# Optimization experiments

Hardware: AMD Instinct MI355X
Metric: run time of the kernel (lower is better)

## Reference

```python
import jax, jax.numpy as jnp
import numpy as np

CH_N = 12
CH_N_CONST = 4
CH_E = 8
MAX_V = 100.0
DT = 1.0


def _build_graph(n_inputs, n_hid, n_actions):
    n_nodes = n_inputs + n_hid + n_actions + 1
    mid = np.arange(n_inputs, n_inputs + n_hid + n_actions)
    src = np.concatenate([
        np.repeat(np.arange(n_inputs), n_hid + n_actions),
        np.repeat(np.arange(n_inputs, n_inputs + n_hid), n_hid + n_actions),
        np.full(n_nodes - 1, n_nodes - 1),
    ])
    tgt = np.concatenate([
        np.tile(mid, n_inputs),
        np.tile(mid, n_hid),
        np.arange(n_nodes - 1),
    ])
    return src.astype(np.int32), tgt.astype(np.int32), n_nodes


def setup_inputs() -> dict:
    n_inputs, n_hid, n_actions, B = 64, 1024, 16, 2
    src, tgt, n_nodes = _build_graph(n_inputs, n_hid, n_actions)
    n_edges = src.shape[0]
    key = jax.random.key(0)
    ks = jax.random.split(key, 10)
    s = 0.05
    d_msg_in = 2 + 2 * CH_N + CH_E          # 34
    d_msg_out = 2 * (CH_N - CH_N_CONST) + CH_E  # 24
    d_upd_in = 3 * CH_N - 2 * CH_N_CONST    # 28
    return {
        "nodes": jax.random.normal(ks[0], (B, n_nodes, CH_N), jnp.float32) * s,
        "edges": jax.random.normal(ks[1], (B, n_edges, CH_E), jnp.float32) * s,
        "msg_w1": jax.random.normal(ks[2], (32, d_msg_in), jnp.float32) * s,
        "msg_b1": jax.random.normal(ks[3], (32,), jnp.float32) * s,
        "msg_w2": jax.random.normal(ks[4], (d_msg_out, 32), jnp.float32) * s,
        "msg_b2": jax.random.normal(ks[5], (d_msg_out,), jnp.float32) * s,
        "upd_w1": jax.random.normal(ks[6], (16, d_upd_in), jnp.float32) * s,
        "upd_b1": jax.random.normal(ks[7], (16,), jnp.float32) * s,
        "upd_w2": jax.random.normal(ks[8], (CH_N - CH_N_CONST, 16), jnp.float32) * s,
        "upd_b2": jax.random.normal(ks[9], (CH_N - CH_N_CONST,), jnp.float32) * s,
        "sources": jnp.asarray(src),
        "targets": jnp.asarray(tgt),
    }


def reference(nodes, edges, msg_w1, msg_b1, msg_w2, msg_b2,
              upd_w1, upd_b1, upd_w2, upd_b2, sources, targets):
    B, N, _ = nodes.shape
    E = edges.shape[1]
    d = CH_N - CH_N_CONST  # dynamic node channels = 8

    # degree features (float for concat)
    out_degs = jax.ops.segment_sum(jnp.ones((E,), nodes.dtype), sources, num_segments=N)
    in_degs = jax.ops.segment_sum(jnp.ones((E,), nodes.dtype), targets, num_segments=N)
    od = jnp.broadcast_to(out_degs[sources][None, :, None], (B, E, 1))
    idg = jnp.broadcast_to(in_degs[targets][None, :, None], (B, E, 1))

    # gather + message MLP: [B, E, 34] -> 32 -> 24
    m_x = jnp.concatenate([nodes[:, sources], nodes[:, targets], edges, od, idg], axis=2)
    h = jax.nn.relu(jnp.einsum('bef,hf->beh', m_x, msg_w1) + msg_b1)
    m = jnp.einsum('beh,oh->beo', h, msg_w2) + msg_b2
    m_a, m_b, m_ab = m[..., :d], m[..., d:2 * d], m[..., 2 * d:]

    # scatter-aggregate (mean)
    agg_a = jnp.zeros((B, N, d), m.dtype).at[:, sources].add(m_a)
    agg_b = jnp.zeros((B, N, d), m.dtype).at[:, targets].add(m_b)
    agg_a = agg_a / jnp.maximum(out_degs, 1.0)[None, :, None]
    agg_b = agg_b / jnp.maximum(in_degs, 1.0)[None, :, None]

    # update MLP: [B, N, 28] -> 16 -> 8
    u_x = jnp.concatenate([agg_a, agg_b, nodes], axis=2)
    uh = jax.nn.relu(jnp.einsum('bnf,hf->bnh', u_x, upd_w1) + upd_b1)
    update = jnp.einsum('bnh,oh->bno', uh, upd_w2) + upd_b2

    # node step (decay=0, set_nodes=False, hard clamp)
    new_dyn = jnp.clip(nodes[..., :d] + update * DT, -MAX_V, MAX_V)
    new_nodes = jnp.concatenate([new_dyn, nodes[..., d:]], axis=-1)
    # edge step (ch_e_const=0, hard clamp)
    new_edges = jnp.clip(edges + m_ab * DT, -MAX_V, MAX_V)
    return new_nodes, new_edges
```

## Files before the change

### kernel.cpp

```cpp
#include <hip/hip_runtime.h>
#include <stdint.h>

#define D_IN1 34
#define H1    32
#define D_OUT1 24
#define D_IN2 28
#define H2    16
#define D_OUT2 8
#define CHN   12
#define CHE   8

__device__ __forceinline__ float clip100(float f) { return fminf(fmaxf(f, -100.f), 100.f); }

__global__ void k_zero(int* __restrict__ p, int n_words) {
    int i = blockIdx.x * blockDim.x + threadIdx.x;
    if (i < n_words) p[i] = 0;
}

__global__ void k_degs(const int* __restrict__ src, const int* __restrict__ tgt,
                       int* __restrict__ outd, int* __restrict__ ind, int E, int N) {
    extern __shared__ int hist[];
    int* ho = hist;
    int* hi = hist + N;
    for (int k = threadIdx.x; k < 2 * N; k += blockDim.x) hist[k] = 0;
    __syncthreads();
    for (int e = blockIdx.x * blockDim.x + threadIdx.x; e < E;
         e += gridDim.x * blockDim.x) {
        int s = src[e];
        int t = tgt[e];
        int s0 = __shfl(s, 0);
        unsigned long long act = __ballot(1);
        if (__all(s == s0)) {
            if ((threadIdx.x & 63) == 0) atomicAdd(&ho[s0], (int)__popcll(act));
        } else {
            atomicAdd(&ho[s], 1);
        }
        atomicAdd(&hi[t], 1);
    }
    __syncthreads();
    for (int k = threadIdx.x; k < N; k += blockDim.x) {
        int a = ho[k], b = hi[k];
        if (a) atomicAdd(&outd[k], a);
        if (b) atomicAdd(&ind[k], b);
    }
}

__launch_bounds__(256)
__global__ void k_pre(const float* __restrict__ nodes,
                      const int* __restrict__ outd, const int* __restrict__ ind,
                      const float* __restrict__ w1, const float* __restrict__ b1,
                      float* __restrict__ SA, float* __restrict__ TB,
                      int N, int total) {
    int i = blockIdx.x * blockDim.x + threadIdx.x;
    if (i >= total) return;
    int n = i % N;

    float x[12];
    const float4* np = (const float4*)(nodes + (size_t)i * CHN);
    float4 n0 = np[0], n1 = np[1], n2 = np[2];
    x[0]=n0.x; x[1]=n0.y; x[2]=n0.z; x[3]=n0.w;
    x[4]=n1.x; x[5]=n1.y; x[6]=n1.z; x[7]=n1.w;
    x[8]=n2.x; x[9]=n2.y; x[10]=n2.z; x[11]=n2.w;
    float od  = (float)outd[n];
    float idg = (float)ind[n];

    float* sap = SA + (size_t)i * H1;
    float* tbp = TB + (size_t)i * H1;
#pragma unroll
    for (int h = 0; h < H1; ++h) {
        const float* wr = w1 + h * D_IN1;
        float a = wr[32] * od;
#pragma unroll
        for (int k = 0; k < 12; ++k) a = fmaf(wr[k], x[k], a);
        sap[h] = a;
        float c = fmaf(wr[33], idg, b1[h]);
#pragma unroll
        for (int k = 0; k < 12; ++k) c = fmaf(wr[12 + k], x[k], c);
        tbp[h] = c;
    }
}

__launch_bounds__(512)
__global__ void k_edge(const float* __restrict__ edges,
                       const float* __restrict__ SA, const float* __restrict__ TB,
                       const float* __restrict__ w1, const float* __restrict__ w2,
                       const float* __restrict__ b2,
                       const int* __restrict__ src, const int* __restrict__ tgt,
                       float* __restrict__ agg_a, float* __restrict__ partials,
                       float* __restrict__ new_edges, int E, int N, int chunk, int nblk_alloc) {
    extern __shared__ float aggB[];
    int blk = blockIdx.x, b = blockIdx.y;
    int start = blk * chunk;
    if (start >= E) return;
    int end = min(E, start + chunk);

    for (int k = threadIdx.x; k < 8 * N; k += 512) aggB[k] = 0.f;
    __syncthreads();

    for (int base = start; base < end; base += 512) {
        int e = base + threadIdx.x;
        bool v = e < end;

        int s = -1, t = -1;
        float ma[8];
        float4 e0, e1;

        if (v) {
            s = src[e];
            t = tgt[e];

            const float4* ep = (const float4*)(edges + ((size_t)b * E + e) * CHE);
            e0 = ep[0]; e1 = ep[1];

            const float4* sap = (const float4*)(SA + ((size_t)b * N + s) * H1);
            const float4* tbp = (const float4*)(TB + ((size_t)b * N + t) * H1);

            float h[H1];
#pragma unroll
            for (int q = 0; q < 8; ++q) {
                float4 a4 = sap[q];
                float4 c4 = tbp[q];
                float hv[4] = { a4.x + c4.x, a4.y + c4.y, a4.z + c4.z, a4.w + c4.w };
#pragma unroll
                for (int r = 0; r < 4; ++r) {
                    const float* wr = w1 + (4 * q + r) * D_IN1 + 24;
                    float a = hv[r];
                    a = fmaf(wr[0], e0.x, a); a = fmaf(wr[1], e0.y, a);
                    a = fmaf(wr[2], e0.z, a); a = fmaf(wr[3], e0.w, a);
                    a = fmaf(wr[4], e1.x, a); a = fmaf(wr[5], e1.y, a);
                    a = fmaf(wr[6], e1.z, a); a = fmaf(wr[7], e1.w, a);
                    h[4 * q + r] = fmaxf(a, 0.f);
                }
            }

#pragma unroll
            for (int o = 0; o < 8; ++o) {
                float a = b2[o];
#pragma unroll
                for (int j = 0; j < H1; ++j) a = fmaf(w2[o * H1 + j], h[j], a);
                ma[o] = a;
            }
#pragma unroll
            for (int o = 0; o < 8; ++o) {
                float a = b2[8 + o];
#pragma unroll
                for (int j = 0; j < H1; ++j) a = fmaf(w2[(8 + o) * H1 + j], h[j], a);
                atomicAdd(&aggB[o * N + t], a);
            }
            float mab[8];
#pragma unroll
            for (int o = 0; o < 8; ++o) {
                float a = b2[16 + o];
#pragma unroll
                for (int j = 0; j < H1; ++j) a = fmaf(w2[(16 + o) * H1 + j], h[j], a);
                mab[o] = a;
            }
            e0.x = clip100(e0.x + mab[0]); e0.y = clip100(e0.y + mab[1]);
            e0.z = clip100(e0.z + mab[2]); e0.w = clip100(e0.w + mab[3]);
            e1.x = clip100(e1.x + mab[4]); e1.y = clip100(e1.y + mab[5]);
            e1.z = clip100(e1.z + mab[6]); e1.w = clip100(e1.w + mab[7]);
            float4* ow = (float4*)(new_edges + ((size_t)b * E + e) * CHE);
            ow[0] = e0; ow[1] = e1;
        }

        int s0 = __shfl(s, 0);
        bool fast = __all(v && s == s0);
        if (fast) {
            float* ga = agg_a + ((size_t)b * N + s0) * 8;
#pragma unroll
            for (int c = 0; c < 8; ++c) {
                float vv = ma[c];
#pragma unroll
                for (int off = 32; off; off >>= 1) vv += __shfl_xor(vv, off);
                if ((threadIdx.x & 63) == 0) atomicAdd(&ga[c], vv);
            }
        } else if (v) {
            float* ga = agg_a + ((size_t)b * N + s) * 8;
#pragma unroll
            for (int c = 0; c < 8; ++c) atomicAdd(&ga[c], ma[c]);
        }
    }

    __syncthreads();
    float* P = partials + ((size_t)b * nblk_alloc + blk) * 8 * N;
    for (int k = threadIdx.x; k < 8 * N; k += 512) P[k] = aggB[k];
}

__global__ void k_aggb(const float* __restrict__ partials, float* __restrict__ agg_b,
                       int nblk_used, int nblk_alloc, int span, int N, int totb) {
    int id = blockIdx.x * blockDim.x + threadIdx.x;
    if (id >= totb) return;
    int p0 = blockIdx.y * span;
    int p1 = min(nblk_used, p0 + span);
    if (p0 >= p1) return;
    int b = id / (8 * N);
    int r = id % (8 * N);
    float sum = 0.f;
    for (int p = p0; p < p1; ++p)
        sum += partials[((size_t)b * nblk_alloc + p) * 8 * N + r];
    atomicAdd(&agg_b[(size_t)b * 8 * N + r], sum);
}

__launch_bounds__(256)
__global__ void k_upd(const float* __restrict__ nodes,
                      const float* __restrict__ agg_a, const float* __restrict__ agg_b,
                      const int* __restrict__ outd, const int* __restrict__ ind,
                      const float* __restrict__ u1, const float* __restrict__ ub1,
                      const float* __restrict__ u2, const float* __restrict__ ub2,
                      float* __restrict__ new_nodes, int N, int total) {
    int i = blockIdx.x * blockDim.x + threadIdx.x;
    if (i >= total) return;
    int b = i / N;
    int n = i % N;

    float rod = 1.f / fmaxf((float)outd[n], 1.f);
    float rdg = 1.f / fmaxf((float)ind[n], 1.f);

    float ux[D_IN2];
    const float4* ga = (const float4*)(agg_a + (size_t)i * 8);
    float4 a0 = ga[0], a1 = ga[1];
    ux[0] = a0.x * rod; ux[1] = a0.y * rod; ux[2] = a0.z * rod; ux[3] = a0.w * rod;
    ux[4] = a1.x * rod; ux[5] = a1.y * rod; ux[6] = a1.z * rod; ux[7] = a1.w * rod;
    const float* gb = agg_b + (size_t)b * 8 * N + n;
#pragma unroll
    for (int c = 0; c < 8; ++c) ux[8 + c] = gb[(size_t)c * N] * rdg;

    const float4* np4 = (const float4*)(nodes + (size_t)i * CHN);
    float4 n0 = np4[0], n1 = np4[1], n2 = np4[2];
    ux[16] = n0.x; ux[17] = n0.y; ux[18] = n0.z; ux[19] = n0.w;
    ux[20] = n1.x; ux[21] = n1.y; ux[22] = n1.z; ux[23] = n1.w;
    ux[24] = n2.x; ux[25] = n2.y; ux[26] = n2.z; ux[27] = n2.w;

    float hb[H2];
#pragma unroll
    for (int h = 0; h < H2; ++h) {
        float a = ub1[h];
#pragma unroll
        for (int k = 0; k < D_IN2; ++k) a = fmaf(u1[h * D_IN2 + k], ux[k], a);
        hb[h] = fmaxf(a, 0.f);
    }
    float up[D_OUT2];
#pragma unroll
    for (int o = 0; o < D_OUT2; ++o) {
        float a = ub2[o];
#pragma unroll
        for (int k = 0; k < H2; ++k) a = fmaf(u2[o * H2 + k], hb[k], a);
        up[o] = clip100(ux[16 + o] + a);
    }
    float4* onp = (float4*)(new_nodes + (size_t)i * CHN);
    onp[0] = make_float4(up[0], up[1], up[2], up[3]);
    onp[1] = make_float4(up[4], up[5], up[6], up[7]);
    onp[2] = n2;
}

extern "C" void kernel_launch(void* const* d_in, const int* in_sizes, int n_in,
                              void* d_out, int out_size, void* d_ws, size_t ws_size,
                              hipStream_t stream) {
    const float* nodes = (const float*)d_in[0];
    const float* edges = (const float*)d_in[1];
    const float* mw1   = (const float*)d_in[2];
    const float* mb1   = (const float*)d_in[3];
    const float* mw2   = (const float*)d_in[4];
    const float* mb2   = (const float*)d_in[5];
    const float* uw1   = (const float*)d_in[6];
    const float* ubb1  = (const float*)d_in[7];
    const float* uw2   = (const float*)d_in[8];
    const float* ubb2  = (const float*)d_in[9];
    const int* src     = (const int*)d_in[10];
    const int* tgt     = (const int*)d_in[11];

    int E = in_sizes[10];
    int B = in_sizes[1] / (E * 8);
    int N = in_sizes[0] / (B * 12);

    size_t off = 0;
    int* outd = (int*)((char*)d_ws + off);       off += (size_t)N * 4;
    int* ind  = (int*)((char*)d_ws + off);       off += (size_t)N * 4;
    off = (off + 63) & ~(size_t)63;
    float* agg_a = (float*)((char*)d_ws + off);  off += (size_t)B * N * 8 * 4;
    float* agg_b = (float*)((char*)d_ws + off);  off += (size_t)B * N * 8 * 4;
    size_t zbytes = off;
    float* SA = (float*)((char*)d_ws + off);     off += (size_t)B * N * H1 * 4;
    float* TB = (float*)((char*)d_ws + off);     off += (size_t)B * N * H1 * 4;
    off = (off + 63) & ~(size_t)63;
    float* partials = (float*)((char*)d_ws + off);

    size_t per_blk = (size_t)B * 8 * N * sizeof(float);
    size_t avail = (ws_size > off) ? (ws_size - off) : 0;
    int nblk = (int)(avail / per_blk);
    if (nblk > 512) nblk = 512;
    if (nblk < 8)   nblk = 8;

    int zwords = (int)(zbytes / 4);
    k_zero<<<(zwords + 255) / 256, 256, 0, stream>>>((int*)d_ws, zwords);

    k_degs<<<256, 256, 2 * N * sizeof(int), stream>>>(src, tgt, outd, ind, E, N);

    int totn = B * N;
    k_pre<<<(totn + 255) / 256, 256, 0, stream>>>(nodes, outd, ind, mw1, mb1,
                                                  SA, TB, N, totn);

    float* out_nodes = (float*)d_out;
    float* out_edges = out_nodes + (size_t)B * N * 12;

    int chunk = (E + nblk - 1) / nblk;
    chunk = (chunk + 511) & ~511;
    int nblk_used = (E + chunk - 1) / chunk;

    dim3 ge(nblk_used, B);
    k_edge<<<ge, 512, 8 * N * sizeof(float), stream>>>(
        edges, SA, TB, mw1, mw2, mb2, src, tgt,
        agg_a, partials, out_edges, E, N, chunk, nblk);

    int totb = B * 8 * N;
    const int P = 16;
    int span = (nblk_used + P - 1) / P;
    dim3 ga((totb + 255) / 256, P);
    k_aggb<<<ga, 256, 0, stream>>>(partials, agg_b, nblk_used, nblk, span, N, totb);

    k_upd<<<(totn + 255) / 256, 256, 0, stream>>>(nodes, agg_a, agg_b, outd, ind,
                                                  uw1, ubb1, uw2, ubb2,
                                                  out_nodes, N, totn);
}
```

Before: 400.0 us.

## Process two edges per thread in edge kernel to share weight loads

Each thread in the edge kernel now handles two consecutive edges. Each weight value is loaded once and applied to both edges, and the source-side hidden vector is read once when the two edges share a source. The wave-level reduction for agg_a now also covers waves that span two distinct sources, so fewer per-lane atomics are issued. The cost is roughly twice the register pressure at a 512-thread launch bound, which risks spills or lower occupancy, and the chunk size is rounded to 1024.

```diff
diff --git a/kernel.cpp b/kernel.cpp
--- a/kernel.cpp
+++ b/kernel.cpp
@@ -3,14 +3,18 @@
 
 #define D_IN1 34
 #define H1    32
-#define D_OUT1 24
 #define D_IN2 28
 #define H2    16
-#define D_OUT2 8
 #define CHN   12
 #define CHE   8
 
 __device__ __forceinline__ float clip100(float f) { return fminf(fmaxf(f, -100.f), 100.f); }
+
+__device__ __forceinline__ float wave_sum64(float v) {
+#pragma unroll
+    for (int off = 32; off; off >>= 1) v += __shfl_xor(v, off);
+    return v;
+}
 
 __global__ void k_zero(int* __restrict__ p, int n_words) {
     int i = blockIdx.x * blockDim.x + threadIdx.x;
@@ -80,6 +84,51 @@
     }
 }
 
+__device__ __forceinline__ void mlp1_one(const float* __restrict__ w1,
+                                         const float4* sap, const float4* tbp,
+                                         const float* x, float* h) {
+#pragma unroll
+    for (int q = 0; q < 8; ++q) {
+        float4 a4 = sap[q], c4 = tbp[q];
+        float hv[4] = { a4.x + c4.x, a4.y + c4.y, a4.z + c4.z, a4.w + c4.w };
+#pragma unroll
+        for (int r = 0; r < 4; ++r) {
+            const float* wr = w1 + (4 * q + r) * D_IN1 + 24;
+            float a = hv[r];
+#pragma unroll
+            for (int k = 0; k < 8; ++k) a = fmaf(wr[k], x[k], a);
+            h[4 * q + r] = fmaxf(a, 0.f);
+        }
+    }
+}
+
+__device__ __forceinline__ void mlp1_pair(const float* __restrict__ w1,
+                                          const float4* sap,
+                                          const float4* tbpA, const float4* tbpB,
+                                          const float* xA, const float* xB,
+                                          float* hA, float* hB) {
+#pragma unroll
+    for (int q = 0; q < 8; ++q) {
+        float4 a4 = sap[q];
+        float4 cA = tbpA[q], cB = tbpB[q];
+        float vA4[4] = { a4.x + cA.x, a4.y + cA.y, a4.z + cA.z, a4.w + cA.w };
+        float vB4[4] = { a4.x + cB.x, a4.y + cB.y, a4.z + cB.z, a4.w + cB.w };
+#pragma unroll
+        for (int r = 0; r < 4; ++r) {
+            const float* wr = w1 + (4 * q + r) * D_IN1 + 24;
+            float aa = vA4[r], ab = vB4[r];
+#pragma unroll
+            for (int k = 0; k < 8; ++k) {
+                float w = wr[k];
+                aa = fmaf(w, xA[k], aa);
+                ab = fmaf(w, xB[k], ab);
+            }
+            hA[4 * q + r] = fmaxf(aa, 0.f);
+            hB[4 * q + r] = fmaxf(ab, 0.f);
+        }
+    }
+}
+
 __launch_bounds__(512)
 __global__ void k_edge(const float* __restrict__ edges,
                        const float* __restrict__ SA, const float* __restrict__ TB,
@@ -97,87 +146,125 @@
     for (int k = threadIdx.x; k < 8 * N; k += 512) aggB[k] = 0.f;
     __syncthreads();
 
-    for (int base = start; base < end; base += 512) {
-        int e = base + threadIdx.x;
-        bool v = e < end;
-
-        int s = -1, t = -1;
-        float ma[8];
-        float4 e0, e1;
-
-        if (v) {
-            s = src[e];
-            t = tgt[e];
-
-            const float4* ep = (const float4*)(edges + ((size_t)b * E + e) * CHE);
-            e0 = ep[0]; e1 = ep[1];
-
-            const float4* sap = (const float4*)(SA + ((size_t)b * N + s) * H1);
-            const float4* tbp = (const float4*)(TB + ((size_t)b * N + t) * H1);
-
-            float h[H1];
-#pragma unroll
-            for (int q = 0; q < 8; ++q) {
-                float4 a4 = sap[q];
-                float4 c4 = tbp[q];
-                float hv[4] = { a4.x + c4.x, a4.y + c4.y, a4.z + c4.z, a4.w + c4.w };
-#pragma unroll
-                for (int r = 0; r < 4; ++r) {
-                    const float* wr = w1 + (4 * q + r) * D_IN1 + 24;
-                    float a = hv[r];
-                    a = fmaf(wr[0], e0.x, a); a = fmaf(wr[1], e0.y, a);
-                    a = fmaf(wr[2], e0.z, a); a = fmaf(wr[3], e0.w, a);
-                    a = fmaf(wr[4], e1.x, a); a = fmaf(wr[5], e1.y, a);
-                    a = fmaf(wr[6], e1.z, a); a = fmaf(wr[7], e1.w, a);
-                    h[4 * q + r] = fmaxf(a, 0.f);
+    float* gab = agg_a + (size_t)b * N * 8;
+
+    for (int base = start; base < end; base += 1024) {
+        int eA = base + 2 * (int)threadIdx.x;
+        int eB = eA + 1;
+        bool vA = eA < end, vB = eB < end;
+
+        int sA = 0, tA = 0, sB = 0, tB = 0;
+        if (vA) { sA = src[eA]; tA = tgt[eA]; }
+        if (vB) { sB = src[eB]; tB = tgt[eB]; }
+
+        float xA[8], xB[8];
+        if (vA) {
+            const float4* ep = (const float4*)(edges + ((size_t)b * E + eA) * CHE);
+            float4 p0 = ep[0], p1 = ep[1];
+            xA[0]=p0.x; xA[1]=p0.y; xA[2]=p0.z; xA[3]=p0.w;
+            xA[4]=p1.x; xA[5]=p1.y; xA[6]=p1.z; xA[7]=p1.w;
+        }
+        if (vB) {
+            const float4* ep = (const float4*)(edges + ((size_t)b * E + eB) * CHE);
+            float4 p0 = ep[0], p1 = ep[1];
+            xB[0]=p0.x; xB[1]=p0.y; xB[2]=p0.z; xB[3]=p0.w;
+            xB[4]=p1.x; xB[5]=p1.y; xB[6]=p1.z; xB[7]=p1.w;
+        }
+
+        const float4* sapA = (const float4*)(SA + ((size_t)b * N + sA) * H1);
+        const float4* tbpA = (const float4*)(TB + ((size_t)b * N + tA) * H1);
+        const float4* tbpB = (const float4*)(TB + ((size_t)b * N + tB) * H1);
+
+        float hA[H1], hB[H1];
+        if (__all(sA == sB)) {
+            mlp1_pair(w1, sapA, tbpA, tbpB, xA, xB, hA, hB);
+        } else {
+            const float4* sapB = (const float4*)(SA + ((size_t)b * N + sB) * H1);
+            mlp1_one(w1, sapA, tbpA, xA, hA);
+            mlp1_one(w1, sapB, tbpB, xB, hB);
+        }
+
+#pragma unroll
+        for (int o = 0; o < 8; ++o) {
+            float aA = b2[16 + o], aB = aA;
+#pragma unroll
+            for (int j = 0; j < H1; ++j) {
+                float w = w2[(16 + o) * H1 + j];
+                aA = fmaf(w, hA[j], aA);
+                aB = fmaf(w, hB[j], aB);
+            }
+            xA[o] = clip100(xA[o] + aA);
+            xB[o] = clip100(xB[o] + aB);
+        }
+        if (vA) {
+            float4* ow = (float4*)(new_edges + ((size_t)b * E + eA) * CHE);
+            ow[0] = make_float4(xA[0], xA[1], xA[2], xA[3]);
+            ow[1] = make_float4(xA[4], xA[5], xA[6], xA[7]);
+        }
+        if (vB) {
+            float4* ow = (float4*)(new_edges + ((size_t)b * E + eB) * CHE);
+            ow[0] = make_float4(xB[0], xB[1], xB[2], xB[3]);
+            ow[1] = make_float4(xB[4], xB[5], xB[6], xB[7]);
+        }
+
+#pragma unroll
+        for (int o = 0; o < 8; ++o) {
+            float aA = b2[8 + o], aB = aA;
+#pragma unroll
+            for (int j = 0; j < H1; ++j) {
+                float w = w2[(8 + o) * H1 + j];
+                aA = fmaf(w, hA[j], aA);
+                aB = fmaf(w, hB[j], aB);
+            }
+            if (vA) atomicAdd(&aggB[o * N + tA], aA);
+            if (vB) atomicAdd(&aggB[o * N + tB], aB);
+        }
+
+        float maA[8], maB[8];
+#pragma unroll
+        for (int o = 0; o < 8; ++o) {
+            float aA = b2[o], aB = aA;
+#pragma unroll
+            for (int j = 0; j < H1; ++j) {
+                float w = w2[o * H1 + j];
+                aA = fmaf(w, hA[j], aA);
+                aB = fmaf(w, hB[j], aB);
+            }
+            maA[o] = aA; maB[o] = aB;
+        }
+
+        int s_lo = __shfl(sA, 0);
+        int s_hi = __shfl(sB, 63);
+        bool valid_all = __all(vA && vB);
+        if (valid_all && __all((sA == s_lo || sA == s_hi) && (sB == s_lo || sB == s_hi))) {
+            if (s_lo == s_hi) {
+#pragma unroll
+                for (int c = 0; c < 8; ++c) {
+                    float vv = wave_sum64(maA[c] + maB[c]);
+                    if ((threadIdx.x & 63) == 0) atomicAdd(&gab[(size_t)s_lo * 8 + c], vv);
                 }
-            }
-
-#pragma unroll
-            for (int o = 0; o < 8; ++o) {
-                float a = b2[o];
-#pragma unroll
-                for (int j = 0; j < H1; ++j) a = fmaf(w2[o * H1 + j], h[j], a);
-                ma[o] = a;
-            }
-#pragma unroll
-            for (int o = 0; o < 8; ++o) {
-                float a = b2[8 + o];
-#pragma unroll
-                for (int j = 0; j < H1; ++j) a = fmaf(w2[(8 + o) * H1 + j], h[j], a);
-                atomicAdd(&aggB[o * N + t], a);
-            }
-            float mab[8];
-#pragma unroll
-            for (int o = 0; o < 8; ++o) {
-                float a = b2[16 + o];
-#pragma unroll
-                for (int j = 0; j < H1; ++j) a = fmaf(w2[(16 + o) * H1 + j], h[j], a);
-                mab[o] = a;
-            }
-            e0.x = clip100(e0.x + mab[0]); e0.y = clip100(e0.y + mab[1]);
-            e0.z = clip100(e0.z + mab[2]); e0.w = clip100(e0.w + mab[3]);
-            e1.x = clip100(e1.x + mab[4]); e1.y = clip100(e1.y + mab[5]);
-            e1.z = clip100(e1.z + mab[6]); e1.w = clip100(e1.w + mab[7]);
-            float4* ow = (float4*)(new_edges + ((size_t)b * E + e) * CHE);
-            ow[0] = e0; ow[1] = e1;
-        }
-
-        int s0 = __shfl(s, 0);
-        bool fast = __all(v && s == s0);
-        if (fast) {
-            float* ga = agg_a + ((size_t)b * N + s0) * 8;
-#pragma unroll
-            for (int c = 0; c < 8; ++c) {
-                float vv = ma[c];
-#pragma unroll
-                for (int off = 32; off; off >>= 1) vv += __shfl_xor(vv, off);
-                if ((threadIdx.x & 63) == 0) atomicAdd(&ga[c], vv);
-            }
-        } else if (v) {
-            float* ga = agg_a + ((size_t)b * N + s) * 8;
-#pragma unroll
-            for (int c = 0; c < 8; ++c) atomicAdd(&ga[c], ma[c]);
+            } else {
+#pragma unroll
+                for (int c = 0; c < 8; ++c) {
+                    float lo = (sA == s_lo ? maA[c] : 0.f) + (sB == s_lo ? maB[c] : 0.f);
+                    float hi = (sA == s_hi ? maA[c] : 0.f) + (sB == s_hi ? maB[c] : 0.f);
+                    lo = wave_sum64(lo);
+                    hi = wave_sum64(hi);
+                    if ((threadIdx.x & 63) == 0) {
+                        atomicAdd(&gab[(size_t)s_lo * 8 + c], lo);
+                        atomicAdd(&gab[(size_t)s_hi * 8 + c], hi);
+                    }
+                }
+            }
+        } else {
+            if (vA) {
+#pragma unroll
+                for (int c = 0; c < 8; ++c) atomicAdd(&gab[(size_t)sA * 8 + c], maA[c]);
+            }
+            if (vB) {
+#pragma unroll
+                for (int c = 0; c < 8; ++c) atomicAdd(&gab[(size_t)sB * 8 + c], maB[c]);
+            }
         }
     }
 
@@ -239,17 +326,16 @@
         for (int k = 0; k < D_IN2; ++k) a = fmaf(u1[h * D_IN2 + k], ux[k], a);
         hb[h] = fmaxf(a, 0.f);
     }
-    float up[D_OUT2];
-#pragma unroll
-    for (int o = 0; o < D_OUT2; ++o) {
+#pragma unroll
+    for (int o = 0; o < 8; ++o) {
         float a = ub2[o];
 #pragma unroll
         for (int k = 0; k < H2; ++k) a = fmaf(u2[o * H2 + k], hb[k], a);
-        up[o] = clip100(ux[16 + o] + a);
+        ux[16 + o] = clip100(ux[16 + o] + a);
     }
     float4* onp = (float4*)(new_nodes + (size_t)i * CHN);
-    onp[0] = make_float4(up[0], up[1], up[2], up[3]);
-    onp[1] = make_float4(up[4], up[5], up[6], up[7]);
+    onp[0] = make_float4(ux[16], ux[17], ux[18], ux[19]);
+    onp[1] = make_float4(ux[20], ux[21], ux[22], ux[23]);
     onp[2] = n2;
 }
 
@@ -304,7 +390,7 @@
     float* out_edges = out_nodes + (size_t)B * N * 12;
 
     int chunk = (E + nblk - 1) / nblk;
-    chunk = (chunk + 511) & ~511;
+    chunk = (chunk + 1023) & ~1023;
     int nblk_used = (E + chunk - 1) / chunk;
 
     dim3 ge(nblk_used, B);
```

After: 421.3 us. 5.3% more time.
